# Kernel optimization log

Hardware: AMD Instinct MI355X
Metric: run time of the kernel (lower is better)

## Reference

```python
import jax, jax.numpy as jnp
import numpy as np

B, N, FIN, FOUT, NMAX = 8, 512, 256, 256, 32
BN_EPS = 1e-5
L2_EPS = 1e-12


def setup_inputs() -> dict:
    key = jax.random.key(0)
    ks = jax.random.split(key, 6)
    x = jax.random.normal(ks[0], (B, N, FIN), dtype=jnp.float32)
    idx1 = jax.random.randint(ks[1], (N * NMAX,), 0, N)
    idx2 = jax.random.randint(ks[2], (N * NMAX,), 0, N)
    idx3 = jax.random.randint(ks[3], (N * NMAX,), 0, N)
    # xavier-ish init for linear weights (torch Linear: y = x @ W.T + b)
    scale = np.sqrt(2.0 / (FIN + FOUT)) * np.sqrt(2.0)
    W_x_w = jax.random.normal(ks[4], (FOUT, FIN), dtype=jnp.float32) * scale
    W_n_w = jax.random.normal(ks[5], (FOUT, FIN), dtype=jnp.float32) * scale
    W_x_b = jnp.zeros((FOUT,), dtype=jnp.float32)
    W_n_b = jnp.zeros((FOUT,), dtype=jnp.float32)
    bn_gamma = jnp.ones((4 * FOUT,), dtype=jnp.float32)
    bn_beta = jnp.zeros((4 * FOUT,), dtype=jnp.float32)
    return {"x": x, "idx1": idx1, "idx2": idx2, "idx3": idx3,
            "W_x_w": W_x_w, "W_x_b": W_x_b, "W_n_w": W_n_w, "W_n_b": W_n_b,
            "bn_gamma": bn_gamma, "bn_beta": bn_beta}


def reference(x, idx1, idx2, idx3, W_x_w, W_x_b, W_n_w, W_n_b, bn_gamma, bn_beta):
    b, n, f = x.shape

    def neib_mean(idx):
        k = idx.shape[0] // n
        g = jnp.take(x, idx, axis=1)            # [B, N*k, F] gather
        return g.reshape(b, n, k, f).mean(axis=2)  # [B, N, F]

    h_self = jnp.einsum('bnf,of->bno', x, W_x_w) + W_x_b
    h1 = jnp.einsum('bnf,of->bno', neib_mean(idx1), W_n_w) + W_n_b
    h2 = jnp.einsum('bnf,of->bno', neib_mean(idx2), W_n_w) + W_n_b
    h3 = jnp.einsum('bnf,of->bno', neib_mean(idx3), W_n_w) + W_n_b
    h = jnp.concatenate([h_self, h1, h2, h3], axis=2)  # [B, N, 4*FOUT]

    # F.normalize(dim=2, p=2): x / max(||x||, eps)
    norm = jnp.sqrt(jnp.sum(h * h, axis=2, keepdims=True))
    h = h / jnp.maximum(norm, L2_EPS)
    h = jax.nn.relu(h)

    # BatchNorm1d over channels (training mode, biased variance), stats over (B, N)
    mu = h.mean(axis=(0, 1))
    var = jnp.mean(jnp.square(h - mu), axis=(0, 1))
    h = (h - mu) * jax.lax.rsqrt(var + BN_EPS) * bn_gamma + bn_beta
    return h
```

## Files before the change

### kernel.cpp

```cpp
#include <hip/hip_runtime.h>
#include <hip/hip_bf16.h>


typedef short  s16x8 __attribute__((ext_vector_type(8)));
typedef float  f32x4 __attribute__((ext_vector_type(4)));
typedef unsigned short u16x4 __attribute__((ext_vector_type(4)));

#define NREP 16
#define P3_ROWS 4

#define OFF_XBF    (0u)
#define OFF_WCAT   (2097152u)
#define OFF_XWX    (2359296u)
#define OFF_XWN    (6553600u)
#define OFF_HBUF   (8650752u)
#define OFF_SUMS   (25427968u)
#define OFF_COEFA  (25559040u)
#define OFF_COEFB  (25563136u)

__device__ __forceinline__ unsigned short f2bf(float f) {
    unsigned int u = __float_as_uint(f);
    u = (u + 0x7FFFu + ((u >> 16) & 1u)) >> 16;
    return (unsigned short)u;
}
__device__ __forceinline__ float bf2f(unsigned short h) {
    return __uint_as_float(((unsigned int)h) << 16);
}

__global__ __launch_bounds__(256) void k0_convert(
    const float* __restrict__ x, const float* __restrict__ Wx,
    const float* __restrict__ Wn,
    unsigned short* __restrict__ x_bf, unsigned short* __restrict__ Wcat)
{
    int e = (blockIdx.x * 256 + threadIdx.x) * 4;
    if (e < 1048576) {
        float4 v = *(const float4*)&x[e];
        u16x4 o; o[0]=f2bf(v.x); o[1]=f2bf(v.y); o[2]=f2bf(v.z); o[3]=f2bf(v.w);
        *(u16x4*)&x_bf[e] = o;
    } else {
        int e2 = e - 1048576;
        if (e2 < 131072) {
            const float* src = (e2 < 65536) ? &Wx[e2] : &Wn[e2 - 65536];
            float4 v = *(const float4*)src;
            u16x4 o; o[0]=f2bf(v.x); o[1]=f2bf(v.y); o[2]=f2bf(v.z); o[3]=f2bf(v.w);
            *(u16x4*)&Wcat[e2] = o;
        }
    }
}

__global__ __launch_bounds__(256) void k1_gemm(
    const unsigned short* __restrict__ A, const unsigned short* __restrict__ W,
    float* __restrict__ xWx, unsigned short* __restrict__ xWn)
{
    const int tid = threadIdx.x;
    const int w = tid >> 6, l = tid & 63;
    const int l15 = l & 15, lhi = l >> 4;
    const int rowBase = blockIdx.x * 64 + w * 16;
    const int colBase = blockIdx.y * 64;

    f32x4 acc[4] = {};
    const unsigned short* ap = &A[(rowBase + l15) * 256 + lhi * 8];
    const unsigned short* wp = &W[(colBase + l15) * 256 + lhi * 8];
    #pragma unroll
    for (int k0 = 0; k0 < 256; k0 += 32) {
        s16x8 a = *(const s16x8*)(ap + k0);
        #pragma unroll
        for (int c = 0; c < 4; ++c) {
            s16x8 b = *(const s16x8*)(wp + c * 16 * 256 + k0);
            acc[c] = __builtin_amdgcn_mfma_f32_16x16x32_bf16(a, b, acc[c], 0, 0, 0);
        }
    }
    const int row0 = rowBase + lhi * 4;
    if (colBase < 256) {
        #pragma unroll
        for (int c = 0; c < 4; ++c)
            #pragma unroll
            for (int r = 0; r < 4; ++r)
                xWx[(row0 + r) * 256 + colBase + c * 16 + l15] = acc[c][r];
    } else {
        #pragma unroll
        for (int c = 0; c < 4; ++c)
            #pragma unroll
            for (int r = 0; r < 4; ++r)
                xWn[(row0 + r) * 256 + (colBase - 256) + c * 16 + l15] = f2bf(acc[c][r]);
    }
}

__global__ __launch_bounds__(256) void k2_rows(
    const float* __restrict__ xWx, const unsigned short* __restrict__ xWn,
    const int* __restrict__ idx1, const int* __restrict__ idx2,
    const int* __restrict__ idx3,
    const float* __restrict__ bx, const float* __restrict__ bn,
    float* __restrict__ hbuf, float* __restrict__ sums)
{
    __shared__ int lidx[96];
    __shared__ float red[4];
    const int t = threadIdx.x;
    const float bxv = bx[t], bnv = bn[t];
    float sA0=0,sA1=0,sA2=0,sA3=0, sQ0=0,sQ1=0,sQ2=0,sQ3=0;

    for (int rr = 0; rr < P3_ROWS; ++rr) {
        const int r = blockIdx.x * P3_ROWS + rr;
        const int b = r >> 9, n = r & 511;
        __syncthreads();
        if (t < 96) {
            int s = t >> 5, k = t & 31;
            const int* ip = (s == 0) ? idx1 : ((s == 1) ? idx2 : idx3);
            lidx[t] = ip[n * 32 + k];
        }
        __syncthreads();
        const unsigned short* base = &xWn[(unsigned)b * (512u * 256u) + (unsigned)t];
        float m1 = 0.f, m2 = 0.f, m3 = 0.f;
        #pragma unroll
        for (int k = 0; k < 32; ++k) m1 += bf2f(base[lidx[k] * 256]);
        #pragma unroll
        for (int k = 0; k < 32; ++k) m2 += bf2f(base[lidx[32 + k] * 256]);
        #pragma unroll
        for (int k = 0; k < 32; ++k) m3 += bf2f(base[lidx[64 + k] * 256]);

        float hs = xWx[r * 256 + t] + bxv;
        float h1 = m1 * (1.f / 32.f) + bnv;
        float h2 = m2 * (1.f / 32.f) + bnv;
        float h3 = m3 * (1.f / 32.f) + bnv;

        float p = hs*hs + h1*h1 + h2*h2 + h3*h3;
        #pragma unroll
        for (int off = 32; off > 0; off >>= 1) p += __shfl_down(p, off);
        if ((t & 63) == 0) red[t >> 6] = p;
        __syncthreads();
        float total = red[0] + red[1] + red[2] + red[3];
        float invn = 1.0f / fmaxf(sqrtf(total), 1e-12f);

        hs = fmaxf(hs * invn, 0.f); h1 = fmaxf(h1 * invn, 0.f);
        h2 = fmaxf(h2 * invn, 0.f); h3 = fmaxf(h3 * invn, 0.f);

        float* hr = &hbuf[(unsigned)r * 1024u];
        hr[t] = hs; hr[256 + t] = h1; hr[512 + t] = h2; hr[768 + t] = h3;

        sA0 += hs; sQ0 += hs*hs;  sA1 += h1; sQ1 += h1*h1;
        sA2 += h2; sQ2 += h2*h2;  sA3 += h3; sQ3 += h3*h3;
    }
    float* sb = &sums[(blockIdx.x & (NREP - 1)) * 2048];
    atomicAdd(&sb[         t], sA0); atomicAdd(&sb[1024 +          t], sQ0);
    atomicAdd(&sb[ 256 +   t], sA1); atomicAdd(&sb[1024 +  256 +   t], sQ1);
    atomicAdd(&sb[ 512 +   t], sA2); atomicAdd(&sb[1024 +  512 +   t], sQ2);
    atomicAdd(&sb[ 768 +   t], sA3); atomicAdd(&sb[1024 +  768 +   t], sQ3);
}

__global__ __launch_bounds__(256) void k3_coef(
    const float* __restrict__ sums, const float* __restrict__ gamma,
    const float* __restrict__ beta, float* __restrict__ cA, float* __restrict__ cB)
{
    int c = blockIdx.x * 256 + threadIdx.x;
    float s = 0.f, s2 = 0.f;
    #pragma unroll
    for (int rep = 0; rep < NREP; ++rep) {
        s  += sums[rep * 2048 + c];
        s2 += sums[rep * 2048 + 1024 + c];
    }
    float mu  = s  * (1.f / 4096.f);
    float var = s2 * (1.f / 4096.f) - mu * mu;
    float a = gamma[c] / sqrtf(var + 1e-5f);
    cA[c] = a;
    cB[c] = beta[c] - mu * a;
}

__global__ __launch_bounds__(256) void k4_apply(
    const float* __restrict__ hbuf, const float* __restrict__ cA,
    const float* __restrict__ cB, float* __restrict__ out)
{
    int gid = blockIdx.x * 256 + threadIdx.x;
    int c0 = (gid & 255) * 4;
    float4 h = *(const float4*)&hbuf[(unsigned)gid * 4u];
    float4 a = *(const float4*)&cA[c0];
    float4 b = *(const float4*)&cB[c0];
    float4 o;
    o.x = h.x * a.x + b.x;  o.y = h.y * a.y + b.y;
    o.z = h.z * a.z + b.z;  o.w = h.w * a.w + b.w;
    *(float4*)&out[(unsigned)gid * 4u] = o;
}

extern "C" void kernel_launch(void* const* d_in, const int* in_sizes, int n_in,
                              void* d_out, int out_size, void* d_ws, size_t ws_size,
                              hipStream_t stream)
{
    const float* x     = (const float*)d_in[0];
    const int*   idx1  = (const int*)  d_in[1];
    const int*   idx2  = (const int*)  d_in[2];
    const int*   idx3  = (const int*)  d_in[3];
    const float* Wx    = (const float*)d_in[4];
    const float* bx    = (const float*)d_in[5];
    const float* Wn    = (const float*)d_in[6];
    const float* bn    = (const float*)d_in[7];
    const float* gamma = (const float*)d_in[8];
    const float* beta  = (const float*)d_in[9];

    char* ws = (char*)d_ws;
    unsigned short* x_bf = (unsigned short*)(ws + OFF_XBF);
    unsigned short* Wcat = (unsigned short*)(ws + OFF_WCAT);
    float*          xWx  = (float*)         (ws + OFF_XWX);
    unsigned short* xWn  = (unsigned short*)(ws + OFF_XWN);
    float*          hbuf = (float*)         (ws + OFF_HBUF);
    float*          sums = (float*)         (ws + OFF_SUMS);
    float*          cA   = (float*)         (ws + OFF_COEFA);
    float*          cB   = (float*)         (ws + OFF_COEFB);

    k0_convert<<<1152, 256, 0, stream>>>(x, Wx, Wn, x_bf, Wcat);
    k1_gemm<<<dim3(64, 8), 256, 0, stream>>>(x_bf, Wcat, xWx, xWn);
    hipMemsetAsync(sums, 0, NREP * 2048 * sizeof(float), stream);
    k2_rows<<<1024, 256, 0, stream>>>(xWx, xWn, idx1, idx2, idx3, bx, bn, hbuf, sums);
    k3_coef<<<4, 256, 0, stream>>>(sums, gamma, beta, cA, cB);
    k4_apply<<<4096, 256, 0, stream>>>(hbuf, cA, cB, (float*)d_out);
}
```

Baseline: 119.4 us.

## Fuse x conversion into GEMM, store intermediates in bf16, drop atomics

Several changes at once. The x-to-bf16 pre-pass is removed: the GEMM now loads fp32 x and converts it in registers, and it also folds the self bias into its output. The self-projection and the normalized h buffer are stored as bf16 instead of fp32, roughly halving intermediate traffic. The row kernel is restructured to one wave per row with vectorized 4-wide gathers, a wave-only norm reduction (no block barrier) and per-block partial sums instead of atomics. This removes the memset, but k3 must now reduce 256 partials, and the bf16 storage of h adds rounding error before BatchNorm.

```diff
diff --git a/kernel.cpp b/kernel.cpp
--- a/kernel.cpp
+++ b/kernel.cpp
@@ -1,56 +1,45 @@
 #include <hip/hip_runtime.h>
-#include <hip/hip_bf16.h>
 
 
 typedef short  s16x8 __attribute__((ext_vector_type(8)));
 typedef float  f32x4 __attribute__((ext_vector_type(4)));
 typedef unsigned short u16x4 __attribute__((ext_vector_type(4)));
 
-#define NREP 16
-#define P3_ROWS 4
-
-#define OFF_XBF    (0u)
-#define OFF_WCAT   (2097152u)
-#define OFF_XWX    (2359296u)
-#define OFF_XWN    (6553600u)
-#define OFF_HBUF   (8650752u)
-#define OFF_SUMS   (25427968u)
-#define OFF_COEFA  (25559040u)
-#define OFF_COEFB  (25563136u)
+#define OFF_WCAT   (0u)
+#define OFF_XWX    (262144u)
+#define OFF_XWN    (2359296u)
+#define OFF_HBUF   (4456448u)
+#define OFF_PART   (12845056u)
+#define OFF_COEFA  (14942208u)
+#define OFF_COEFB  (14946304u)
 
 __device__ __forceinline__ unsigned short f2bf(float f) {
     unsigned int u = __float_as_uint(f);
     u = (u + 0x7FFFu + ((u >> 16) & 1u)) >> 16;
     return (unsigned short)u;
 }
-__device__ __forceinline__ float bf2f(unsigned short h) {
-    return __uint_as_float(((unsigned int)h) << 16);
+__device__ __forceinline__ float bflo(unsigned int d) {
+    return __uint_as_float(d << 16);
+}
+__device__ __forceinline__ float bfhi(unsigned int d) {
+    return __uint_as_float(d & 0xFFFF0000u);
 }
 
 __global__ __launch_bounds__(256) void k0_convert(
-    const float* __restrict__ x, const float* __restrict__ Wx,
-    const float* __restrict__ Wn,
-    unsigned short* __restrict__ x_bf, unsigned short* __restrict__ Wcat)
+    const float* __restrict__ Wx, const float* __restrict__ Wn,
+    unsigned short* __restrict__ Wcat)
 {
     int e = (blockIdx.x * 256 + threadIdx.x) * 4;
-    if (e < 1048576) {
-        float4 v = *(const float4*)&x[e];
-        u16x4 o; o[0]=f2bf(v.x); o[1]=f2bf(v.y); o[2]=f2bf(v.z); o[3]=f2bf(v.w);
-        *(u16x4*)&x_bf[e] = o;
-    } else {
-        int e2 = e - 1048576;
-        if (e2 < 131072) {
-            const float* src = (e2 < 65536) ? &Wx[e2] : &Wn[e2 - 65536];
-            float4 v = *(const float4*)src;
-            u16x4 o; o[0]=f2bf(v.x); o[1]=f2bf(v.y); o[2]=f2bf(v.z); o[3]=f2bf(v.w);
-            *(u16x4*)&Wcat[e2] = o;
-        }
-    }
+    const float* src = (e < 65536) ? &Wx[e] : &Wn[e - 65536];
+    float4 v = *(const float4*)src;
+    u16x4 o; o[0]=f2bf(v.x); o[1]=f2bf(v.y); o[2]=f2bf(v.z); o[3]=f2bf(v.w);
+    *(u16x4*)&Wcat[e] = o;
 }
 
 __global__ __launch_bounds__(256) void k1_gemm(
-    const unsigned short* __restrict__ A, const unsigned short* __restrict__ W,
-    float* __restrict__ xWx, unsigned short* __restrict__ xWn)
+    const float* __restrict__ x, const unsigned short* __restrict__ W,
+    const float* __restrict__ bx,
+    unsigned short* __restrict__ xWx, unsigned short* __restrict__ xWn)
 {
     const int tid = threadIdx.x;
     const int w = tid >> 6, l = tid & 63;
@@ -59,24 +48,32 @@
     const int colBase = blockIdx.y * 64;
 
     f32x4 acc[4] = {};
-    const unsigned short* ap = &A[(rowBase + l15) * 256 + lhi * 8];
+    const float*          ap = &x[(rowBase + l15) * 256 + lhi * 8];
     const unsigned short* wp = &W[(colBase + l15) * 256 + lhi * 8];
     #pragma unroll
-    for (int k0 = 0; k0 < 256; k0 += 32) {
-        s16x8 a = *(const s16x8*)(ap + k0);
+    for (int kk = 0; kk < 256; kk += 32) {
+        float4 a0 = *(const float4*)(ap + kk);
+        float4 a1 = *(const float4*)(ap + kk + 4);
+        s16x8 a;
+        a[0]=(short)f2bf(a0.x); a[1]=(short)f2bf(a0.y);
+        a[2]=(short)f2bf(a0.z); a[3]=(short)f2bf(a0.w);
+        a[4]=(short)f2bf(a1.x); a[5]=(short)f2bf(a1.y);
+        a[6]=(short)f2bf(a1.z); a[7]=(short)f2bf(a1.w);
         #pragma unroll
         for (int c = 0; c < 4; ++c) {
-            s16x8 b = *(const s16x8*)(wp + c * 16 * 256 + k0);
+            s16x8 b = *(const s16x8*)(wp + c * 16 * 256 + kk);
             acc[c] = __builtin_amdgcn_mfma_f32_16x16x32_bf16(a, b, acc[c], 0, 0, 0);
         }
     }
     const int row0 = rowBase + lhi * 4;
     if (colBase < 256) {
         #pragma unroll
-        for (int c = 0; c < 4; ++c)
+        for (int c = 0; c < 4; ++c) {
+            float bxv = bx[colBase + c * 16 + l15];
             #pragma unroll
             for (int r = 0; r < 4; ++r)
-                xWx[(row0 + r) * 256 + colBase + c * 16 + l15] = acc[c][r];
+                xWx[(row0 + r) * 256 + colBase + c * 16 + l15] = f2bf(acc[c][r] + bxv);
+        }
     } else {
         #pragma unroll
         for (int c = 0; c < 4; ++c)
@@ -87,76 +84,107 @@
 }
 
 __global__ __launch_bounds__(256) void k2_rows(
-    const float* __restrict__ xWx, const unsigned short* __restrict__ xWn,
+    const unsigned short* __restrict__ xWx, const unsigned short* __restrict__ xWn,
     const int* __restrict__ idx1, const int* __restrict__ idx2,
-    const int* __restrict__ idx3,
-    const float* __restrict__ bx, const float* __restrict__ bn,
-    float* __restrict__ hbuf, float* __restrict__ sums)
-{
-    __shared__ int lidx[96];
-    __shared__ float red[4];
-    const int t = threadIdx.x;
-    const float bxv = bx[t], bnv = bn[t];
-    float sA0=0,sA1=0,sA2=0,sA3=0, sQ0=0,sQ1=0,sQ2=0,sQ3=0;
-
-    for (int rr = 0; rr < P3_ROWS; ++rr) {
-        const int r = blockIdx.x * P3_ROWS + rr;
+    const int* __restrict__ idx3, const float* __restrict__ bn,
+    unsigned short* __restrict__ hbuf, float* __restrict__ part)
+{
+    __shared__ int   lidx[4][96];
+    __shared__ float lpart[4][2048];
+    const int t = threadIdx.x, w = t >> 6, l = t & 63;
+    const float4 bnv = *(const float4*)&bn[l * 4];
+    f32x4 sA[4] = {}, sQ[4] = {};
+
+    #pragma unroll 1
+    for (int rr = 0; rr < 4; ++rr) {
+        const int r = blockIdx.x * 16 + w * 4 + rr;
         const int b = r >> 9, n = r & 511;
         __syncthreads();
-        if (t < 96) {
-            int s = t >> 5, k = t & 31;
-            const int* ip = (s == 0) ? idx1 : ((s == 1) ? idx2 : idx3);
-            lidx[t] = ip[n * 32 + k];
+        if (l < 32) {
+            lidx[w][l]      = idx1[n * 32 + l];
+            lidx[w][64 + l] = idx3[n * 32 + l];
+        } else {
+            lidx[w][l]      = idx2[n * 32 + (l & 31)];
         }
         __syncthreads();
-        const unsigned short* base = &xWn[(unsigned)b * (512u * 256u) + (unsigned)t];
-        float m1 = 0.f, m2 = 0.f, m3 = 0.f;
-        #pragma unroll
-        for (int k = 0; k < 32; ++k) m1 += bf2f(base[lidx[k] * 256]);
-        #pragma unroll
-        for (int k = 0; k < 32; ++k) m2 += bf2f(base[lidx[32 + k] * 256]);
-        #pragma unroll
-        for (int k = 0; k < 32; ++k) m3 += bf2f(base[lidx[64 + k] * 256]);
-
-        float hs = xWx[r * 256 + t] + bxv;
-        float h1 = m1 * (1.f / 32.f) + bnv;
-        float h2 = m2 * (1.f / 32.f) + bnv;
-        float h3 = m3 * (1.f / 32.f) + bnv;
-
-        float p = hs*hs + h1*h1 + h2*h2 + h3*h3;
-        #pragma unroll
-        for (int off = 32; off > 0; off >>= 1) p += __shfl_down(p, off);
-        if ((t & 63) == 0) red[t >> 6] = p;
-        __syncthreads();
-        float total = red[0] + red[1] + red[2] + red[3];
-        float invn = 1.0f / fmaxf(sqrtf(total), 1e-12f);
-
-        hs = fmaxf(hs * invn, 0.f); h1 = fmaxf(h1 * invn, 0.f);
-        h2 = fmaxf(h2 * invn, 0.f); h3 = fmaxf(h3 * invn, 0.f);
-
-        float* hr = &hbuf[(unsigned)r * 1024u];
-        hr[t] = hs; hr[256 + t] = h1; hr[512 + t] = h2; hr[768 + t] = h3;
-
-        sA0 += hs; sQ0 += hs*hs;  sA1 += h1; sQ1 += h1*h1;
-        sA2 += h2; sQ2 += h2*h2;  sA3 += h3; sQ3 += h3*h3;
-    }
-    float* sb = &sums[(blockIdx.x & (NREP - 1)) * 2048];
-    atomicAdd(&sb[         t], sA0); atomicAdd(&sb[1024 +          t], sQ0);
-    atomicAdd(&sb[ 256 +   t], sA1); atomicAdd(&sb[1024 +  256 +   t], sQ1);
-    atomicAdd(&sb[ 512 +   t], sA2); atomicAdd(&sb[1024 +  512 +   t], sQ2);
-    atomicAdd(&sb[ 768 +   t], sA3); atomicAdd(&sb[1024 +  768 +   t], sQ3);
+
+        const unsigned short* basep = &xWn[(unsigned)b * (512u * 256u)];
+        f32x4 m1 = {}, m2 = {}, m3 = {};
+        #pragma unroll
+        for (int k = 0; k < 32; ++k) {
+            uint2 d = *(const uint2*)(basep + lidx[w][k] * 256 + l * 4);
+            m1[0] += bflo(d.x); m1[1] += bfhi(d.x);
+            m1[2] += bflo(d.y); m1[3] += bfhi(d.y);
+        }
+        #pragma unroll
+        for (int k = 0; k < 32; ++k) {
+            uint2 d = *(const uint2*)(basep + lidx[w][32 + k] * 256 + l * 4);
+            m2[0] += bflo(d.x); m2[1] += bfhi(d.x);
+            m2[2] += bflo(d.y); m2[3] += bfhi(d.y);
+        }
+        #pragma unroll
+        for (int k = 0; k < 32; ++k) {
+            uint2 d = *(const uint2*)(basep + lidx[w][64 + k] * 256 + l * 4);
+            m3[0] += bflo(d.x); m3[1] += bfhi(d.x);
+            m3[2] += bflo(d.y); m3[3] += bfhi(d.y);
+        }
+
+        uint2 hd = *(const uint2*)(xWx + r * 256 + l * 4);
+        f32x4 hseg[4];
+        hseg[0][0] = bflo(hd.x); hseg[0][1] = bfhi(hd.x);
+        hseg[0][2] = bflo(hd.y); hseg[0][3] = bfhi(hd.y);
+        #pragma unroll
+        for (int j = 0; j < 4; ++j) {
+            hseg[1][j] = m1[j] * (1.f / 32.f) + bnv[j];
+            hseg[2][j] = m2[j] * (1.f / 32.f) + bnv[j];
+            hseg[3][j] = m3[j] * (1.f / 32.f) + bnv[j];
+        }
+        float p = 0.f;
+        #pragma unroll
+        for (int s = 0; s < 4; ++s)
+            #pragma unroll
+            for (int j = 0; j < 4; ++j) p += hseg[s][j] * hseg[s][j];
+        #pragma unroll
+        for (int m = 32; m > 0; m >>= 1) p += __shfl_xor(p, m);
+        const float invn = 1.0f / fmaxf(sqrtf(p), 1e-12f);
+
+        unsigned short* hr = &hbuf[(unsigned)r * 1024u];
+        #pragma unroll
+        for (int s = 0; s < 4; ++s) {
+            f32x4 v;
+            #pragma unroll
+            for (int j = 0; j < 4; ++j) v[j] = fmaxf(hseg[s][j] * invn, 0.f);
+            uint2 o;
+            o.x = (unsigned)f2bf(v[0]) | ((unsigned)f2bf(v[1]) << 16);
+            o.y = (unsigned)f2bf(v[2]) | ((unsigned)f2bf(v[3]) << 16);
+            *(uint2*)(hr + s * 256 + l * 4) = o;
+            #pragma unroll
+            for (int j = 0; j < 4; ++j) { sA[s][j] += v[j]; sQ[s][j] += v[j]*v[j]; }
+        }
+    }
+    #pragma unroll
+    for (int s = 0; s < 4; ++s)
+        #pragma unroll
+        for (int j = 0; j < 4; ++j) {
+            lpart[w][       s * 256 + l * 4 + j] = sA[s][j];
+            lpart[w][1024 + s * 256 + l * 4 + j] = sQ[s][j];
+        }
+    __syncthreads();
+    for (int c = t; c < 2048; c += 256)
+        part[blockIdx.x * 2048 + c] =
+            lpart[0][c] + lpart[1][c] + lpart[2][c] + lpart[3][c];
 }
 
 __global__ __launch_bounds__(256) void k3_coef(
-    const float* __restrict__ sums, const float* __restrict__ gamma,
+    const float* __restrict__ part, const float* __restrict__ gamma,
     const float* __restrict__ beta, float* __restrict__ cA, float* __restrict__ cB)
 {
     int c = blockIdx.x * 256 + threadIdx.x;
     float s = 0.f, s2 = 0.f;
-    #pragma unroll
-    for (int rep = 0; rep < NREP; ++rep) {
-        s  += sums[rep * 2048 + c];
-        s2 += sums[rep * 2048 + 1024 + c];
+    #pragma unroll 32
+    for (int rep = 0; rep < 256; ++rep) {
+        s  += part[rep * 2048 + c];
+        s2 += part[rep * 2048 + 1024 + c];
     }
     float mu  = s  * (1.f / 4096.f);
     float var = s2 * (1.f / 4096.f) - mu * mu;
@@ -166,17 +194,17 @@
 }
 
 __global__ __launch_bounds__(256) void k4_apply(
-    const float* __restrict__ hbuf, const float* __restrict__ cA,
+    const unsigned short* __restrict__ hbuf, const float* __restrict__ cA,
     const float* __restrict__ cB, float* __restrict__ out)
 {
     int gid = blockIdx.x * 256 + threadIdx.x;
     int c0 = (gid & 255) * 4;
-    float4 h = *(const float4*)&hbuf[(unsigned)gid * 4u];
+    uint2 hd = *(const uint2*)(hbuf + (unsigned)gid * 4u);
     float4 a = *(const float4*)&cA[c0];
     float4 b = *(const float4*)&cB[c0];
     float4 o;
-    o.x = h.x * a.x + b.x;  o.y = h.y * a.y + b.y;
-    o.z = h.z * a.z + b.z;  o.w = h.w * a.w + b.w;
+    o.x = bflo(hd.x) * a.x + b.x;  o.y = bfhi(hd.x) * a.y + b.y;
+    o.z = bflo(hd.y) * a.z + b.z;  o.w = bfhi(hd.y) * a.w + b.w;
     *(float4*)&out[(unsigned)gid * 4u] = o;
 }
 
@@ -196,19 +224,17 @@
     const float* beta  = (const float*)d_in[9];
 
     char* ws = (char*)d_ws;
-    unsigned short* x_bf = (unsigned short*)(ws + OFF_XBF);
     unsigned short* Wcat = (unsigned short*)(ws + OFF_WCAT);
-    float*          xWx  = (float*)         (ws + OFF_XWX);
+    unsigned short* xWx  = (unsigned short*)(ws + OFF_XWX);
     unsigned short* xWn  = (unsigned short*)(ws + OFF_XWN);
-    float*          hbuf = (float*)         (ws + OFF_HBUF);
-    float*          sums = (float*)         (ws + OFF_SUMS);
+    unsigned short* hbuf = (unsigned short*)(ws + OFF_HBUF);
+    float*          part = (float*)         (ws + OFF_PART);
     float*          cA   = (float*)         (ws + OFF_COEFA);
     float*          cB   = (float*)         (ws + OFF_COEFB);
 
-    k0_convert<<<1152, 256, 0, stream>>>(x, Wx, Wn, x_bf, Wcat);
-    k1_gemm<<<dim3(64, 8), 256, 0, stream>>>(x_bf, Wcat, xWx, xWn);
-    hipMemsetAsync(sums, 0, NREP * 2048 * sizeof(float), stream);
-    k2_rows<<<1024, 256, 0, stream>>>(xWx, xWn, idx1, idx2, idx3, bx, bn, hbuf, sums);
-    k3_coef<<<4, 256, 0, stream>>>(sums, gamma, beta, cA, cB);
+    k0_convert<<<128, 256, 0, stream>>>(Wx, Wn, Wcat);
+    k1_gemm<<<dim3(64, 8), 256, 0, stream>>>(x, Wcat, bx, xWx, xWn);
+    k2_rows<<<256, 256, 0, stream>>>(xWx, xWn, idx1, idx2, idx3, bn, hbuf, part);
+    k3_coef<<<4, 256, 0, stream>>>(part, gamma, beta, cA, cB);
     k4_apply<<<4096, 256, 0, stream>>>(hbuf, cA, cB, (float*)d_out);
 }
```

Result: slower. 181.9 us (+52.4%).
